# Performance work log

Measured on AMD Instinct MI355X. Metric: run time of the kernel, lower is better.

The kernel has to match this reference:

```python
import jax, jax.numpy as jnp
import numpy as np

BATCH_SIZE = 4096
HYPER_LAMBDA = 0.5
EMBED_DIM = 512


def setup_inputs() -> dict:
    key = jax.random.key(0)
    k1, k2 = jax.random.split(key)
    emb_i = jax.random.normal(k1, (BATCH_SIZE, EMBED_DIM), dtype=jnp.float32)
    emb_j = jax.random.normal(k2, (BATCH_SIZE, EMBED_DIM), dtype=jnp.float32)
    return {"emb_i": emb_i, "emb_j": emb_j}


def reference(emb_i, emb_j):
    n = emb_i.shape[0]  # batch_size
    lam = jnp.asarray(HYPER_LAMBDA, dtype=emb_i.dtype)
    # L2-normalize rows (F.normalize, dim=1)
    z_i = emb_i / jnp.linalg.norm(emb_i, axis=1, keepdims=True)
    z_j = emb_j / jnp.linalg.norm(emb_j, axis=1, keepdims=True)
    reps = jnp.concatenate([z_i, z_j], axis=0)  # [2N, D]
    # cosine similarity of already-normalized rows == dot product
    sim = reps @ reps.T  # [2N, 2N]
    # diagonals at offsets +N and -N: sim[k, k+N] and sim[k+N, k]
    idx = jnp.arange(n)
    sim_ij = sim[idx, idx + n]
    sim_ji = sim[idx + n, idx]
    positives = jnp.concatenate([sim_ij, sim_ji], axis=0)  # [2N]
    positives_similarity = jnp.log1p(jnp.exp(-positives + lam))
    neg_mask = 1.0 - jnp.eye(2 * n, dtype=sim.dtype)
    negatives_exp = neg_mask * jnp.exp(sim - lam)
    negatives_similarity = jnp.log1p(negatives_exp)
    positives_sum = jnp.sum(positives_similarity) / (2 * n)
    negatives_sum = jnp.sum(negatives_similarity) / (12 * n)
    return positives_sum + negatives_sum
```

## Files before the change

### kernel.cpp

```cpp
#include <hip/hip_runtime.h>
#include <hip/hip_bf16.h>
#include <hip/hip_fp8.h>
#include <math.h>

typedef float floatx4 __attribute__((ext_vector_type(4)));
typedef long long i64;
typedef long long i64x2 __attribute__((ext_vector_type(2)));

#define N_ROWS 4096
#define DIM 512
#define LAM 0.5f
#define NT 64
#define NTILES (NT * (NT + 1) / 2)
#define GRID 512

#define GLOBAL_AS(p) ((const __attribute__((address_space(1))) void*)(p))
#define LDS_AS(p) ((__attribute__((address_space(3))) void*)(p))

__device__ __forceinline__ unsigned int pack4_fp8(float a, float b, float c, float d) {
    unsigned int u0 = __hip_cvt_float_to_fp8(a, __HIP_SATFINITE, __HIP_E4M3);
    unsigned int u1 = __hip_cvt_float_to_fp8(b, __HIP_SATFINITE, __HIP_E4M3);
    unsigned int u2 = __hip_cvt_float_to_fp8(c, __HIP_SATFINITE, __HIP_E4M3);
    unsigned int u3 = __hip_cvt_float_to_fp8(d, __HIP_SATFINITE, __HIP_E4M3);
    return u0 | (u1 << 8) | (u2 << 16) | (u3 << 24);
}

__global__ __launch_bounds__(256) void normalize_kernel(
    const float* __restrict__ ei, const float* __restrict__ ej,
    unsigned char* __restrict__ Z, float* __restrict__ out) {
    if (blockIdx.x == 0 && threadIdx.x == 0) out[0] = 0.0f;
    const int w = threadIdx.x >> 6, lane = threadIdx.x & 63;
    const int row = blockIdx.x * 4 + w;
    const float* __restrict__ src = (row < N_ROWS)
        ? (ei + (size_t)row * DIM)
        : (ej + (size_t)(row - N_ROWS) * DIM);
    const float4* src4 = (const float4*)src;
    float4 v0 = src4[lane];
    float4 v1 = src4[lane + 64];
    float s = v0.x*v0.x + v0.y*v0.y + v0.z*v0.z + v0.w*v0.w
            + v1.x*v1.x + v1.y*v1.y + v1.z*v1.z + v1.w*v1.w;
    #pragma unroll
    for (int off = 32; off; off >>= 1) s += __shfl_xor(s, off);
    const float r = rsqrtf(s);

    __shared__ __align__(16) unsigned char buf[4][512];
    ((unsigned int*)buf[w])[lane]      = pack4_fp8(v0.x*r, v0.y*r, v0.z*r, v0.w*r);
    ((unsigned int*)buf[w])[lane + 64] = pack4_fp8(v1.x*r, v1.y*r, v1.z*r, v1.w*r);
    __syncthreads();

    const int kt = lane >> 3, q = (lane >> 1) & 3, h = lane & 1;
    i64 val = *(const i64*)(buf[w] + kt * 64 + h * 32 + q * 8);
    const int p = (kt * 4 + q) ^ (row & 3);
    *(i64*)(Z + (size_t)row * DIM + p * 16 + h * 8) = val;
}

__global__ __launch_bounds__(256, 2) void simloss_kernel(
    const unsigned char* __restrict__ Z, float* __restrict__ out) {
    const int tid = threadIdx.x;
    const int w = tid >> 6, lane = tid & 63;
    const int q = lane >> 4, m16 = lane & 15;
    const int wm = w & 1, wn = w >> 1;

    __shared__ __align__(16) unsigned char As[3][128 * 64];
    __shared__ __align__(16) unsigned char Bs[3][128 * 64];
    __shared__ float red[4];

    const int fragSwz = m16 & 3;
    const int stRow = w * 32 + (lane >> 2);
    const int stCol = (lane & 3) * 16;
    const int ldsOff = w * 2048;

    const int bid = blockIdx.x;
    const int nMine = 4 + ((bid & 15) == 0);

    auto decode = [](int id, int& bm, int& bn) {
        int m = (int)((2*NT + 1 - sqrtf((float)((2*NT+1)*(2*NT+1)) - 8.0f * (float)id)) * 0.5f);
        if (m < 0) m = 0; if (m > NT-1) m = NT-1;
        while ((m + 1) * NT - ((m + 1) * m) / 2 <= id) ++m;
        while (m * NT - (m * (m - 1)) / 2 > id) --m;
        bm = m;
        bn = m + (id - (m * NT - (m * (m - 1)) / 2));
    };
    auto tileIdx = [bid](int mt) {
        return (mt < 4) ? (bid + mt * GRID) : (4 * GRID + (bid >> 4));
    };

    int bm, bn; decode(tileIdx(0), bm, bn);
    const unsigned char* stA = Z + (size_t)(bm * 128 + stRow) * DIM + stCol;
    const unsigned char* stB = Z + (size_t)(bn * 128 + stRow) * DIM + stCol;

    float negsum = 0.0f, possum = 0.0f;

    #define ISSUE(b, pA, pB, kOff)                                               \
        _Pragma("unroll")                                                        \
        for (int l = 0; l < 2; ++l) {                                            \
            __builtin_amdgcn_global_load_lds(GLOBAL_AS((pA) + (size_t)l * 16 * DIM + (kOff)), \
                                             LDS_AS(&As[b][ldsOff + l * 1024]), 16, 0, 0); \
            __builtin_amdgcn_global_load_lds(GLOBAL_AS((pB) + (size_t)l * 16 * DIM + (kOff)), \
                                             LDS_AS(&Bs[b][ldsOff + l * 1024]), 16, 0, 0); \
        }

    ISSUE(0, stA, stB, 0)
    ISSUE(1, stA, stB, 64)

    for (int mt = 0; mt < nMine; ++mt) {
        const bool hasNext = (mt + 1 < nMine);
        int nbm = 0, nbn = 0;
        const unsigned char *nA = stA, *nB = stB;
        if (hasNext) {
            decode(tileIdx(mt + 1), nbm, nbn);
            nA = Z + (size_t)(nbm * 128 + stRow) * DIM + stCol;
            nB = Z + (size_t)(nbn * 128 + stRow) * DIM + stCol;
        }

        floatx4 acc[4][4] = {};

        #pragma unroll
        for (int u = 0; u < 8; ++u) {
            const int g = mt * 8 + u;
            const int b = g % 3;
            if (u == 7 && !hasNext) { asm volatile("s_waitcnt vmcnt(0)" ::: "memory"); }
            else                    { asm volatile("s_waitcnt vmcnt(4)" ::: "memory"); }
            __builtin_amdgcn_sched_barrier(0);
            __builtin_amdgcn_s_barrier();
            if (u < 6)         { ISSUE((g + 2) % 3, stA, stB, (u + 2) * 64) }
            else if (hasNext)  { ISSUE((g + 2) % 3, nA, nB, (u - 6) * 64) }

            const unsigned char* fraA = &As[b][(wm * 64 + m16) * 64];
            const unsigned char* fraB = &Bs[b][(wn * 64 + m16) * 64];
            const int cOff = (q ^ fragSwz) << 4;
            i64x2 af[4], bf[4];
            #pragma unroll
            for (int i = 0; i < 4; ++i) af[i] = *(const i64x2*)(fraA + i * 16 * 64 + cOff);
            #pragma unroll
            for (int j = 0; j < 4; ++j) bf[j] = *(const i64x2*)(fraB + j * 16 * 64 + cOff);
            __builtin_amdgcn_s_setprio(1);
            #pragma unroll
            for (int i = 0; i < 4; ++i)
                #pragma unroll
                for (int j = 0; j < 4; ++j)
                    acc[i][j] = __builtin_amdgcn_mfma_f32_16x16x32_fp8_fp8(af[i].x, bf[j].x, acc[i][j], 0, 0, 0);
            #pragma unroll
            for (int i = 0; i < 4; ++i)
                #pragma unroll
                for (int j = 0; j < 4; ++j)
                    acc[i][j] = __builtin_amdgcn_mfma_f32_16x16x32_fp8_fp8(af[i].y, bf[j].y, acc[i][j], 0, 0, 0);
            __builtin_amdgcn_s_setprio(0);
        }

        const int tm = bm * 2 + wm, tn = bn * 2 + wn;
        const float wgt = (tn < tm) ? 0.0f : ((tn == tm) ? 1.0f : 2.0f);
        const bool hasPos = (tn == tm + 64);
        if (wgt != 0.0f) {
            const int rowBase = tm * 64 + q * 4;
            const int colBase = tn * 64 + m16;
            float nacc = 0.0f;
            #pragma unroll
            for (int j = 0; j < 4; ++j) {
                const int cg = colBase + j * 16;
                float p = 1.0f;
                #pragma unroll
                for (int i = 0; i < 4; ++i) {
                    const int rg0 = rowBase + i * 16;
                    #pragma unroll
                    for (int r = 0; r < 4; ++r) {
                        const float sv = acc[i][j][r];
                        float e = __expf(sv - LAM);
                        if (rg0 + r == cg) e = 0.0f;
                        p *= (1.0f + e);
                        if (hasPos && cg == rg0 + r + N_ROWS)
                            possum += log1pf(expf(-sv + LAM));
                    }
                }
                nacc += __logf(p);
            }
            negsum += nacc * wgt;
        }

        bm = nbm; bn = nbn; stA = nA; stB = nB;
    }

    #pragma unroll
    for (int off = 32; off; off >>= 1) {
        negsum += __shfl_xor(negsum, off);
        possum += __shfl_xor(possum, off);
    }
    const float part = negsum * (1.0f / (12.0f * (float)N_ROWS))
                     + possum * (1.0f / (float)N_ROWS);
    if (lane == 0) red[w] = part;
    __syncthreads();
    if (tid == 0) atomicAdd(out, red[0] + red[1] + red[2] + red[3]);
    #undef ISSUE
}

extern "C" void kernel_launch(void* const* d_in, const int* in_sizes, int n_in,
                              void* d_out, int out_size, void* d_ws, size_t ws_size,
                              hipStream_t stream) {
    const float* ei = (const float*)d_in[0];
    const float* ej = (const float*)d_in[1];
    float* out = (float*)d_out;
    unsigned char* Z = (unsigned char*)d_ws;

    normalize_kernel<<<2048, 256, 0, stream>>>(ei, ej, Z, out);
    simloss_kernel<<<GRID, 256, 0, stream>>>(Z, out);
}
```

Before: 106.4 us.

## Give each wave private LDS staging to drop block barriers in GEMM loop

Each wave now loads its own 64-row A and B slices into a private LDS region, using a double buffer instead of the shared triple buffer. Because a wave only reads data it loaded itself, the per-k-step s_barrier is removed and only vmcnt waits remain. The cost is duplicated global/L2 traffic (each A/B slice is loaded by two waves) and a shallower prefetch depth. The rewritten wait count and buffer index look consistent, but the wave-local correctness relies on the ordering that vmcnt alone provides.

```diff
diff --git a/kernel.cpp b/kernel.cpp
--- a/kernel.cpp
+++ b/kernel.cpp
@@ -61,14 +61,13 @@
     const int q = lane >> 4, m16 = lane & 15;
     const int wm = w & 1, wn = w >> 1;
 
-    __shared__ __align__(16) unsigned char As[3][128 * 64];
-    __shared__ __align__(16) unsigned char Bs[3][128 * 64];
+    __shared__ __align__(16) unsigned char As[2][4][4096];
+    __shared__ __align__(16) unsigned char Bs[2][4][4096];
     __shared__ float red[4];
 
     const int fragSwz = m16 & 3;
-    const int stRow = w * 32 + (lane >> 2);
+    const int stRow = lane >> 2;
     const int stCol = (lane & 3) * 16;
-    const int ldsOff = w * 2048;
 
     const int bid = blockIdx.x;
     const int nMine = 4 + ((bid & 15) == 0);
@@ -86,22 +85,21 @@
     };
 
     int bm, bn; decode(tileIdx(0), bm, bn);
-    const unsigned char* stA = Z + (size_t)(bm * 128 + stRow) * DIM + stCol;
-    const unsigned char* stB = Z + (size_t)(bn * 128 + stRow) * DIM + stCol;
+    const unsigned char* stA = Z + (size_t)(bm * 128 + wm * 64 + stRow) * DIM + stCol;
+    const unsigned char* stB = Z + (size_t)(bn * 128 + wn * 64 + stRow) * DIM + stCol;
 
     float negsum = 0.0f, possum = 0.0f;
 
     #define ISSUE(b, pA, pB, kOff)                                               \
         _Pragma("unroll")                                                        \
-        for (int l = 0; l < 2; ++l) {                                            \
+        for (int l = 0; l < 4; ++l) {                                            \
             __builtin_amdgcn_global_load_lds(GLOBAL_AS((pA) + (size_t)l * 16 * DIM + (kOff)), \
-                                             LDS_AS(&As[b][ldsOff + l * 1024]), 16, 0, 0); \
+                                             LDS_AS(&As[b][w][l * 1024]), 16, 0, 0); \
             __builtin_amdgcn_global_load_lds(GLOBAL_AS((pB) + (size_t)l * 16 * DIM + (kOff)), \
-                                             LDS_AS(&Bs[b][ldsOff + l * 1024]), 16, 0, 0); \
+                                             LDS_AS(&Bs[b][w][l * 1024]), 16, 0, 0); \
         }
 
     ISSUE(0, stA, stB, 0)
-    ISSUE(1, stA, stB, 64)
 
     for (int mt = 0; mt < nMine; ++mt) {
         const bool hasNext = (mt + 1 < nMine);
@@ -109,31 +107,29 @@
         const unsigned char *nA = stA, *nB = stB;
         if (hasNext) {
             decode(tileIdx(mt + 1), nbm, nbn);
-            nA = Z + (size_t)(nbm * 128 + stRow) * DIM + stCol;
-            nB = Z + (size_t)(nbn * 128 + stRow) * DIM + stCol;
+            nA = Z + (size_t)(nbm * 128 + wm * 64 + stRow) * DIM + stCol;
+            nB = Z + (size_t)(nbn * 128 + wn * 64 + stRow) * DIM + stCol;
         }
 
         floatx4 acc[4][4] = {};
 
         #pragma unroll
         for (int u = 0; u < 8; ++u) {
-            const int g = mt * 8 + u;
-            const int b = g % 3;
+            const int b = u & 1;
+            if (u < 7)        { ISSUE(b ^ 1, stA, stB, (u + 1) * 64) }
+            else if (hasNext) { ISSUE(b ^ 1, nA, nB, 0) }
             if (u == 7 && !hasNext) { asm volatile("s_waitcnt vmcnt(0)" ::: "memory"); }
-            else                    { asm volatile("s_waitcnt vmcnt(4)" ::: "memory"); }
+            else                    { asm volatile("s_waitcnt vmcnt(8)" ::: "memory"); }
             __builtin_amdgcn_sched_barrier(0);
-            __builtin_amdgcn_s_barrier();
-            if (u < 6)         { ISSUE((g + 2) % 3, stA, stB, (u + 2) * 64) }
-            else if (hasNext)  { ISSUE((g + 2) % 3, nA, nB, (u - 6) * 64) }
-
-            const unsigned char* fraA = &As[b][(wm * 64 + m16) * 64];
-            const unsigned char* fraB = &Bs[b][(wn * 64 + m16) * 64];
+
+            const unsigned char* fraA = &As[b][w][m16 * 64];
+            const unsigned char* fraB = &Bs[b][w][m16 * 64];
             const int cOff = (q ^ fragSwz) << 4;
             i64x2 af[4], bf[4];
             #pragma unroll
-            for (int i = 0; i < 4; ++i) af[i] = *(const i64x2*)(fraA + i * 16 * 64 + cOff);
-            #pragma unroll
-            for (int j = 0; j < 4; ++j) bf[j] = *(const i64x2*)(fraB + j * 16 * 64 + cOff);
+            for (int i = 0; i < 4; ++i) af[i] = *(const i64x2*)(fraA + i * 1024 + cOff);
+            #pragma unroll
+            for (int j = 0; j < 4; ++j) bf[j] = *(const i64x2*)(fraB + j * 1024 + cOff);
             __builtin_amdgcn_s_setprio(1);
             #pragma unroll
             for (int i = 0; i < 4; ++i)
```

After: 105.9 us. No clear change (-0.5%).
